# Optimization experiments

Measured on AMD Instinct MI355X. Metric: run time of the kernel, lower is better.

The kernel has to match this reference:

```python
import jax, jax.numpy as jnp
import numpy as np

D = 256
HID = 128
TOPK = 100
NEG = -20.0


def setup_inputs() -> dict:
    key = jax.random.key(0)
    ks = jax.random.split(key, 10)
    B, Ll, Lp = 2, 96, 768
    l_tok = jax.random.normal(ks[0], (B, Ll, D), dtype=jnp.float32)
    p_tok = jax.random.normal(ks[1], (B, Lp, D), dtype=jnp.float32)
    # trailing-position padding (pad last 8 ligand / 64 protein tokens)
    l_pad = jnp.broadcast_to(jnp.arange(Ll) >= Ll - 8, (B, Ll))
    p_pad = jnp.broadcast_to(jnp.arange(Lp) >= Lp - 64, (B, Lp))
    s = 0.02
    Wl = jax.random.normal(ks[2], (D, D), dtype=jnp.float32) * s
    bl = jnp.zeros((D,), jnp.float32)
    Wp = jax.random.normal(ks[3], (D, D), dtype=jnp.float32) * s
    bp = jnp.zeros((D,), jnp.float32)
    W1 = jax.random.normal(ks[4], (4 * D, HID), dtype=jnp.float32) * s
    b1 = jnp.zeros((HID,), jnp.float32)
    W2 = jax.random.normal(ks[5], (HID, HID), dtype=jnp.float32) * s
    b2 = jnp.zeros((HID,), jnp.float32)
    W3 = jax.random.normal(ks[6], (HID, 1), dtype=jnp.float32) * s
    b3 = jnp.zeros((1,), jnp.float32)
    return {"l_tok": l_tok, "p_tok": p_tok, "l_pad": l_pad, "p_pad": p_pad,
            "Wl": Wl, "bl": bl, "Wp": Wp, "bp": bp,
            "W1": W1, "b1": b1, "W2": W2, "b2": b2, "W3": W3, "b3": b3}


def _pair_head(l_tok, p_tok, l_pad, p_pad, Wl, bl, Wp, bp, W1, b1, W2, b2, W3, b3):
    B, Ll, d = l_tok.shape
    Lp = p_tok.shape[1]
    l = l_tok @ Wl + bl                      # [B,Ll,D]
    p = p_tok @ Wp + bp                      # [B,Lp,D]
    le = jnp.broadcast_to(l[:, :, None, :], (B, Ll, Lp, d))
    pe = jnp.broadcast_to(p[:, None, :, :], (B, Ll, Lp, d))
    pair = jnp.concatenate([le, pe, le * pe, jnp.abs(le - pe)], axis=-1)  # [B,Ll,Lp,4D]
    h = jax.nn.gelu(pair @ W1 + b1, approximate=False)
    h = jax.nn.gelu(h @ W2 + b2, approximate=False)
    logit_map = (h @ W3 + b3)[..., 0]        # [B,Ll,Lp]
    logit_map = jnp.nan_to_num(logit_map, nan=0.0, posinf=20.0, neginf=NEG)
    valid = (~l_pad)[:, :, None] & (~p_pad)[:, None, :]
    logit_map = jnp.where(valid, logit_map, NEG)
    flat = logit_map.reshape(B, Ll * Lp)
    k = min(TOPK, Ll * Lp)
    topv, _ = jax.lax.top_k(flat, k)
    w = jax.nn.softmax(topv, axis=-1)
    return jnp.sum(w * topv, axis=-1)        # [B]


def reference(l_tok, p_tok, l_pad, p_pad, Wl, bl, Wp, bp, W1, b1, W2, b2, W3, b3):
    return _pair_head(l_tok, p_tok, l_pad, p_pad, Wl, bl, Wp, bp, W1, b1, W2, b2, W3, b3)
```

## Files before the change

### kernel.cpp

```cpp
#include <hip/hip_runtime.h>
#include <hip/hip_bf16.h>
#include <math.h>

#define LL 96
#define LP 768
#define BD 256
#define HD 128
#define NB 2
#define NEGV (-20.0f)
#define LB 8
#define PB 16

#define NBIN 4096
#define BSHIFT 20
#define CAP 8192
#define NLOG (LL * LP)

typedef __attribute__((ext_vector_type(4))) float f32x4;
typedef __attribute__((ext_vector_type(4))) unsigned int u32x4;
typedef __attribute__((ext_vector_type(8))) short s16x8;

__device__ __forceinline__ float gelu_fast(float x) {
  float ax = fabsf(x) * 0.70710678118654752f;
  float t = __builtin_amdgcn_rcpf(fmaf(0.3275911f, ax, 1.0f));
  float poly = t * fmaf(t, fmaf(t, fmaf(t, fmaf(t, 1.061405429f, -1.453152027f),
                                        1.421413741f), -0.284496736f), 0.254829592f);
  float e = __expf(-ax * ax);
  float erfax = fmaf(-poly, e, 1.0f);
  float erfx = copysignf(erfax, x);
  return 0.5f * x * (1.0f + erfx);
}

__device__ __forceinline__ f32x4 mfma16(s16x8 a, s16x8 b, f32x4 c) {
  return __builtin_amdgcn_mfma_f32_16x16x32_bf16(a, b, c, 0, 0, 0);
}

__device__ __forceinline__ unsigned pack_bf16(float a, float b) {
  float2 t; t.x = a; t.y = b;
  __hip_bfloat162 h = __float22bfloat162_rn(t);
  return *reinterpret_cast<unsigned*>(&h);
}

__device__ __forceinline__ s16x8 as_s16x8(u32x4 v) {
  return __builtin_bit_cast(s16x8, v);
}

__device__ __forceinline__ s16x8 pack8(f32x4 x0, f32x4 x1) {
  u32x4 v;
  v[0] = pack_bf16(x0[0], x0[1]);
  v[1] = pack_bf16(x0[2], x0[3]);
  v[2] = pack_bf16(x1[0], x1[1]);
  v[3] = pack_bf16(x1[2], x1[3]);
  return as_s16x8(v);
}

__device__ __forceinline__ unsigned short bfbits(float x) {
  __hip_bfloat16 h = __float2bfloat16(x);
  return *reinterpret_cast<unsigned short*>(&h);
}

__device__ __forceinline__ unsigned int fkey(float f) {
  unsigned int u = __float_as_uint(f);
  return u ^ ((u >> 31) ? 0xFFFFFFFFu : 0x80000000u);
}
__device__ __forceinline__ float finv(unsigned int k) {
  unsigned int u = k ^ ((k >> 31) ? 0x80000000u : 0xFFFFFFFFu);
  return __uint_as_float(u);
}


__global__ __launch_bounds__(256) void prep_kernel(
    const void* lp, const void* pp, unsigned char* lmask, unsigned char* pmask,
    const float* __restrict__ W1, const float* __restrict__ W2,
    unsigned short* __restrict__ W1xf, unsigned short* __restrict__ W2f,
    const float* __restrict__ l_tok, const float* __restrict__ p_tok,
    const float* __restrict__ Wl, const float* __restrict__ bl,
    const float* __restrict__ Wp, const float* __restrict__ bp,
    const float* __restrict__ b1,
    float* __restrict__ wl_, float* __restrict__ wp_,
    float* __restrict__ wA, float* __restrict__ wB,
    unsigned* __restrict__ zero_base) {
  __shared__ int bad;
  const int tid = threadIdx.x;
  if (blockIdx.x == 0) {
    for (int i = tid; i < NB * NBIN + 32; i += 256) zero_base[i] = 0u;
    if (tid == 0) bad = 0;
    __syncthreads();
    const unsigned int* li = (const unsigned int*)lp;
    const unsigned int* pi = (const unsigned int*)pp;
    for (int i = tid; i < NB * LL; i += 256) if (li[i] > 1u) atomicOr(&bad, 1);
    for (int i = tid; i < NB * LP; i += 256) if (pi[i] > 1u) atomicOr(&bad, 1);
    __syncthreads();
    const bool asInt = (bad == 0);
    const unsigned char* lb = (const unsigned char*)lp;
    const unsigned char* pb = (const unsigned char*)pp;
    for (int i = tid; i < NB * LL; i += 256)
      lmask[i] = asInt ? (unsigned char)(li[i] != 0u) : (unsigned char)(lb[i] != 0);
    for (int i = tid; i < NB * LP; i += 256)
      pmask[i] = asInt ? (unsigned char)(pi[i] != 0u) : (unsigned char)(pb[i] != 0);
    return;
  }
  if (blockIdx.x < 321) {
    int idx = (blockIdx.x - 1) * 256 + tid;
    if (idx < 65536) {
      int j = idx & 7, ln = (idx >> 3) & 63;
      int rest = idx >> 9;
      int mt = rest & 7, kt = (rest >> 3) & 1, cc = rest >> 4;
      int row = 512 + cc * 64 + kt * 32 + ((ln >> 4) << 3) + j;
      int col = mt * 16 + (ln & 15);
      W1xf[idx] = bfbits(W1[row * HD + col]);
    } else if (idx < 65536 + 16384) {
      int e = idx - 65536;
      int j = e & 7, ln = (e >> 3) & 63, mt = (e >> 9) & 7, kt = e >> 12;
      int row = kt * 32 + ((ln >> 4) << 3) + j;
      int col = mt * 16 + (ln & 15);
      W2f[e] = bfbits(W2[row * HD + col]);
    }
    return;
  }
  const int pblk = blockIdx.x - 321;
  const bool isL = pblk < (NB * LL / 16);
  const int blk = isL ? pblk : (pblk - NB * LL / 16);
  const int r0 = blk * 16;
  const float* X = isL ? l_tok : p_tok;
  const float* W = isL ? Wl : Wp;
  const float* bias = isL ? bl : bp;
  float* Y1 = isL ? wl_ : wp_;
  float* Y2 = isL ? wA : wB;
  const float* W1p = isL ? W1 : (W1 + 256 * HD);

  const int lane = tid & 63;
  const int wv = tid >> 6;
  const int mrow = lane & 15;
  const int kg = (lane >> 4) * 8;
  const int drow = (lane >> 4) * 4;

  f32x4 accA[4];
#pragma unroll
  for (int q = 0; q < 4; ++q) {
    float bv = bias[(wv * 4 + q) * 16 + mrow];
    accA[q] = (f32x4){bv, bv, bv, bv};
  }
#pragma unroll
  for (int kt = 0; kt < 8; ++kt) {
    const float* xr = &X[(size_t)(r0 + mrow) * 256 + kt * 32 + kg];
    s16x8 af = pack8(*(const f32x4*)xr, *(const f32x4*)(xr + 4));
#pragma unroll
    for (int q = 0; q < 4; ++q) {
      const int nc = (wv * 4 + q) * 16 + mrow;
      f32x4 w0, w1;
#pragma unroll
      for (int j = 0; j < 4; ++j) {
        w0[j] = W[(size_t)(kt * 32 + kg + j) * 256 + nc];
        w1[j] = W[(size_t)(kt * 32 + kg + 4 + j) * 256 + nc];
      }
      accA[q] = mfma16(af, pack8(w0, w1), accA[q]);
    }
  }
#pragma unroll
  for (int q = 0; q < 4; ++q)
#pragma unroll
    for (int r = 0; r < 4; ++r)
      Y1[(size_t)(r0 + drow + r) * 256 + (wv * 4 + q) * 16 + mrow] = accA[q][r];
  __syncthreads();

  f32x4 accB[2];
#pragma unroll
  for (int q = 0; q < 2; ++q) {
    float bv = isL ? b1[(wv * 2 + q) * 16 + mrow] : 0.0f;
    accB[q] = (f32x4){bv, bv, bv, bv};
  }
#pragma unroll
  for (int kt = 0; kt < 8; ++kt) {
    const float* yr = &Y1[(size_t)(r0 + mrow) * 256 + kt * 32 + kg];
    s16x8 af = pack8(*(const f32x4*)yr, *(const f32x4*)(yr + 4));
#pragma unroll
    for (int q = 0; q < 2; ++q) {
      const int nc = (wv * 2 + q) * 16 + mrow;
      f32x4 w0, w1;
#pragma unroll
      for (int j = 0; j < 4; ++j) {
        w0[j] = W1p[(size_t)(kt * 32 + kg + j) * HD + nc];
        w1[j] = W1p[(size_t)(kt * 32 + kg + 4 + j) * HD + nc];
      }
      accB[q] = mfma16(af, pack8(w0, w1), accB[q]);
    }
  }
#pragma unroll
  for (int q = 0; q < 2; ++q)
#pragma unroll
    for (int r = 0; r < 4; ++r)
      Y2[(size_t)(r0 + drow + r) * HD + (wv * 2 + q) * 16 + mrow] = accB[q][r];
}

__global__ __launch_bounds__(256, 3) void pair2_kernel(
    const float* __restrict__ lbuf, const float* __restrict__ pbuf,
    const float* __restrict__ A1, const float* __restrict__ B1,
    const unsigned short* __restrict__ W1xf, const unsigned short* __restrict__ W2f,
    const float* __restrict__ b2, const float* __restrict__ W3,
    const float* __restrict__ b3, const unsigned char* __restrict__ lmask,
    const unsigned char* __restrict__ pmask, float* __restrict__ logits) {
  __shared__ float U[8192];

  const int tid = threadIdx.x;
  const int lane = tid & 63;
  const int w = tid >> 6;
  const int g = lane >> 4;
  const int c = lane & 15;
  const int bb = blockIdx.z;
  const int i0 = blockIdx.y * LB;
  const int j0 = blockIdx.x * PB;

  float* lt0 = U;
  float* lt1 = U + 1632;

  const int srow = tid >> 4, sq = tid & 15;
  const int srow2 = (tid + 256) >> 4;

  auto gaddr = [&](int row, int q, int c4) -> const float* {
    return (row < 8)
        ? &lbuf[(size_t)(bb * LL + i0 + row) * BD + c4 * 64 + q * 4]
        : &pbuf[(size_t)(bb * LP + j0 + (row - 8)) * BD + c4 * 64 + q * 4];
  };

  {
    f32x4 r0 = *(const f32x4*)gaddr(srow, sq, 0);
    f32x4 r1 = {};
    if (tid < 128) r1 = *(const f32x4*)gaddr(srow2, sq, 0);
    *(f32x4*)&lt0[srow * 68 + sq * 4] = r0;
    if (tid < 128) *(f32x4*)&lt0[srow2 * 68 + sq * 4] = r1;
  }
  __syncthreads();

  f32x4 acc1[8][2];
#pragma unroll
  for (int m = 0; m < 8; ++m)
#pragma unroll
    for (int n = 0; n < 2; ++n) acc1[m][n] = (f32x4)0.0f;

  for (int c4 = 0; c4 < 4; ++c4) {
    float* cur = (c4 & 1) ? lt1 : lt0;
    float* nxt = (c4 & 1) ? lt0 : lt1;

    f32x4 r0 = {}, r1 = {};
    if (c4 < 3) {
      r0 = *(const f32x4*)gaddr(srow, sq, c4 + 1);
      if (tid < 128) r1 = *(const f32x4*)gaddr(srow2, sq, c4 + 1);
    }

#pragma unroll
    for (int kt = 0; kt < 2; ++kt) {
      const int kc0 = kt * 32 + g * 8;
      s16x8 a0[8];
#pragma unroll
      for (int m = 0; m < 8; ++m)
        a0[m] = *(const s16x8*)(W1xf +
            ((size_t)((c4 * 2 + kt) * 8 + m) * 64 + lane) * 8);

      const f32x4 p0 = *(const f32x4*)&cur[(8 + c) * 68 + kc0];
      const f32x4 p1 = *(const f32x4*)&cur[(8 + c) * 68 + kc0 + 4];
      s16x8 bf0[2], bf1[2];
#pragma unroll
      for (int n = 0; n < 2; ++n) {
        const int ntg = w * 2 + n;
        const f32x4 l0 = *(const f32x4*)&cur[ntg * 68 + kc0];
        const f32x4 l1 = *(const f32x4*)&cur[ntg * 68 + kc0 + 4];
        u32x4 bv;
        bv[0] = pack_bf16(l0[0] * p0[0], l0[1] * p0[1]);
        bv[1] = pack_bf16(l0[2] * p0[2], l0[3] * p0[3]);
        bv[2] = pack_bf16(l1[0] * p1[0], l1[1] * p1[1]);
        bv[3] = pack_bf16(l1[2] * p1[2], l1[3] * p1[3]);
        bf0[n] = as_s16x8(bv);
      }

      s16x8 a1[8];
#pragma unroll
      for (int m = 0; m < 8; ++m)
        a1[m] = *(const s16x8*)(W1xf +
            ((size_t)(((4 + c4) * 2 + kt) * 8 + m) * 64 + lane) * 8);

#pragma unroll
      for (int n = 0; n < 2; ++n) {
        const int ntg = w * 2 + n;
        const f32x4 l0 = *(const f32x4*)&cur[ntg * 68 + kc0];
        const f32x4 l1 = *(const f32x4*)&cur[ntg * 68 + kc0 + 4];
        u32x4 bv;
        bv[0] = pack_bf16(fabsf(l0[0] - p0[0]), fabsf(l0[1] - p0[1]));
        bv[1] = pack_bf16(fabsf(l0[2] - p0[2]), fabsf(l0[3] - p0[3]));
        bv[2] = pack_bf16(fabsf(l1[0] - p1[0]), fabsf(l1[1] - p1[1]));
        bv[3] = pack_bf16(fabsf(l1[2] - p1[2]), fabsf(l1[3] - p1[3]));
        bf1[n] = as_s16x8(bv);
      }

#pragma unroll
      for (int m = 0; m < 8; ++m) {
        acc1[m][0] = mfma16(a0[m], bf0[0], acc1[m][0]);
        acc1[m][1] = mfma16(a0[m], bf0[1], acc1[m][1]);
      }
#pragma unroll
      for (int m = 0; m < 8; ++m) {
        acc1[m][0] = mfma16(a1[m], bf1[0], acc1[m][0]);
        acc1[m][1] = mfma16(a1[m], bf1[1], acc1[m][1]);
      }
    }

    if (c4 < 3) {
      *(f32x4*)&nxt[srow * 68 + sq * 4] = r0;
      if (tid < 128) *(f32x4*)&nxt[srow2 * 68 + sq * 4] = r1;
    }
    __syncthreads();
  }

  unsigned* Hdw = (unsigned*)U;
#pragma unroll
  for (int m = 0; m < 8; ++m) {
    const int kt2 = (4 * m + g) >> 3;
    const int l2 = ((2 * m + (g >> 1)) & 3) * 16 + c;
    const int jd = (g & 1) * 2;
    const f32x4 b1v = *(const f32x4*)&B1[(size_t)(bb * LP + j0 + c) * HD + m * 16 + g * 4];
#pragma unroll
    for (int n = 0; n < 2; ++n) {
      const int ntg = w * 2 + n;
      f32x4 a1v = *(const f32x4*)&A1[(size_t)(bb * LL + i0 + ntg) * HD + m * 16 + g * 4];
      float h0 = gelu_fast(acc1[m][n][0] + a1v[0] + b1v[0]);
      float h1 = gelu_fast(acc1[m][n][1] + a1v[1] + b1v[1]);
      float h2 = gelu_fast(acc1[m][n][2] + a1v[2] + b1v[2]);
      float h3 = gelu_fast(acc1[m][n][3] + a1v[3] + b1v[3]);
      uint2 hw;
      hw.x = pack_bf16(h0, h1);
      hw.y = pack_bf16(h2, h3);
      *(uint2*)&Hdw[((kt2 * 8 + ntg) * 64 + l2) * 4 + jd] = hw;
    }
  }
  __syncthreads();

  f32x4 acc2[8][2];
#pragma unroll
  for (int m = 0; m < 8; ++m)
#pragma unroll
    for (int n = 0; n < 2; ++n) acc2[m][n] = (f32x4)0.0f;

  const unsigned short* Hush = (const unsigned short*)U;
#pragma unroll
  for (int kt = 0; kt < 4; ++kt) {
    s16x8 a2[8];
#pragma unroll
    for (int m = 0; m < 8; ++m)
      a2[m] = *(const s16x8*)(W2f + (size_t)((kt * 8 + m) * 64 + lane) * 8);
    s16x8 bf[2];
#pragma unroll
    for (int n = 0; n < 2; ++n)
      bf[n] = *((const s16x8*)Hush + ((kt * 8 + (w * 2 + n)) * 64 + lane));
#pragma unroll
    for (int m = 0; m < 8; ++m) {
      acc2[m][0] = mfma16(a2[m], bf[0], acc2[m][0]);
      acc2[m][1] = mfma16(a2[m], bf[1], acc2[m][1]);
    }
  }

  float partial[2] = {0.0f, 0.0f};
#pragma unroll
  for (int m = 0; m < 8; ++m) {
    const int hb = m * 16 + g * 4;
    f32x4 b2v = *(const f32x4*)&b2[hb];
    f32x4 w3v = *(const f32x4*)&W3[hb];
#pragma unroll
    for (int n = 0; n < 2; ++n) {
#pragma unroll
      for (int r = 0; r < 4; ++r)
        partial[n] = fmaf(gelu_fast(acc2[m][n][r] + b2v[r]), w3v[r], partial[n]);
    }
  }
#pragma unroll
  for (int n = 0; n < 2; ++n) {
    partial[n] += __shfl_xor(partial[n], 16, 64);
    partial[n] += __shfl_xor(partial[n], 32, 64);
  }
  if (g == 0) {
    const float bb3 = b3[0];
#pragma unroll
    for (int n = 0; n < 2; ++n) {
      const int ntg = w * 2 + n;
      float v = partial[n] + bb3;
      if (isnan(v)) v = 0.0f;
      else if (isinf(v)) v = (v > 0.0f) ? 20.0f : NEGV;
      const int i = i0 + ntg, j = j0 + c;
      if (lmask[bb * LL + i] || pmask[bb * LP + j]) v = NEGV;
      logits[(size_t)bb * NLOG + i * LP + j] = v;
    }
  }
}

__global__ __launch_bounds__(256) void topk_kernel(const float* __restrict__ logits,
                                                   unsigned* __restrict__ hist,
                                                   unsigned* __restrict__ ctrl,
                                                   float* __restrict__ cand,
                                                   float* __restrict__ out) {
  __shared__ unsigned lh[NBIN];
  __shared__ unsigned csum[256];
  __shared__ unsigned suf[256];
  __shared__ unsigned topb[256];
  __shared__ float red[256];
  __shared__ unsigned sP, sN, isLastS;
  __shared__ unsigned bc[8];
  const int b = blockIdx.y;
  const int tid = threadIdx.x;
  const float* data = logits + (size_t)b * NLOG;
  const int stride = gridDim.x * 256;

  for (int i = tid; i < NBIN; i += 256) lh[i] = 0u;
  __syncthreads();
  for (int i = blockIdx.x * 256 + tid; i < NLOG; i += stride)
    atomicAdd(&lh[fkey(data[i]) >> BSHIFT], 1u);
  __syncthreads();
  unsigned* gh = hist + b * NBIN;
  for (int i = tid; i < NBIN; i += 256) {
    unsigned v = lh[i];
    if (v) atomicAdd(&gh[i], v);
  }
  __threadfence();
  if (tid == 0) isLastS = (atomicAdd(&ctrl[12 + b], 1u) == gridDim.x - 1);
  __syncthreads();

  if (isLastS) {
    __threadfence();
    const int base = tid * (NBIN / 256);
    unsigned s = 0;
    int top = -1;
    for (int i = 0; i < NBIN / 256; ++i) {
      unsigned cnt = gh[base + i];
      s += cnt;
      if (cnt) top = base + i;
    }
    csum[tid] = s;
    topb[tid] = (unsigned)(top + 1);
    __syncthreads();
    if (tid == 0) {
      unsigned a = 0;
      for (int t = 255; t >= 0; --t) { suf[t] = a; a += csum[t]; }
      unsigned mt = 0;
      for (int t = 0; t < 256; ++t) mt = max(mt, topb[t]);
      ctrl[b] = ((mt - 1u) << BSHIFT) | ((1u << BSHIFT) - 1u);
    }
    __syncthreads();
    unsigned above = suf[tid];
    if (above < 100u && above + csum[tid] >= 100u) {
      unsigned a = above;
      for (int i = NBIN / 256 - 1; i >= 0; --i) {
        unsigned hc = gh[base + i];
        if (a + hc >= 100u) { ctrl[4 + b] = base + i; ctrl[6 + b] = a; break; }
        a += hc;
      }
    }
    __syncthreads();
    __threadfence();
    if (tid == 0) atomicExch(&ctrl[16 + b], 1u);
  } else {
    if (tid == 0) {
      int guard = 0;
      while (atomicAdd(&ctrl[16 + b], 0u) == 0u && guard < (1 << 24)) {
        __builtin_amdgcn_s_sleep(32);
        ++guard;
      }
    }
    __syncthreads();
  }

  if (tid == 0) {
    bc[0] = atomicAdd(&ctrl[4 + b], 0u);
    bc[1] = atomicAdd(&ctrl[b], 0u);
  }
  __syncthreads();
  const unsigned B = bc[0];
  const float vmax = finv(bc[1]);

  {
    float l1 = 0.0f, l2 = 0.0f;
    for (int i = blockIdx.x * 256 + tid; i < NLOG; i += stride) {
      float v = data[i];
      unsigned kb = fkey(v) >> BSHIFT;
      if (kb > B) {
        float e = __expf(v - vmax);
        l1 += e;
        l2 = fmaf(e, v, l2);
      } else if (kb == B) {
        unsigned pos = atomicAdd(&ctrl[2 + b], 1u);
        if (pos < CAP) cand[(size_t)b * CAP + pos] = v;
      }
    }
    if (l1 != 0.0f) {
      atomicAdd((float*)&ctrl[8 + b], l1);
      atomicAdd((float*)&ctrl[10 + b], l2);
    }
  }
  __threadfence();
  if (tid == 0) isLastS = (atomicAdd(&ctrl[14 + b], 1u) == gridDim.x - 1);
  __syncthreads();
  if (!isLastS) return;
  __threadfence();

  if (tid == 0) {
    bc[2] = atomicAdd(&ctrl[2 + b], 0u);
    bc[3] = atomicAdd(&ctrl[6 + b], 0u);
    bc[4] = __float_as_uint(atomicAdd((float*)&ctrl[8 + b], 0.0f));
    bc[5] = __float_as_uint(atomicAdd((float*)&ctrl[10 + b], 0.0f));
  }
  __syncthreads();
  const unsigned count = bc[2];
  const unsigned G = bc[3];
  const float s1g = __uint_as_float(bc[4]);
  const float s2g = __uint_as_float(bc[5]);
  const float* cv = cand + (size_t)b * CAP;
  const bool fb = count > CAP;
  const unsigned C = fb ? 0u : count;

  if (tid == 0) { sP = 0u; sN = fb ? 100u : (100u - G); }
  __syncthreads();

  for (int sh = 24; sh >= 0; sh -= 8) {
    csum[tid] = 0u;
    __syncthreads();
    const unsigned prefix = sP;
    const unsigned maskhi = (sh == 24) ? 0u : (0xFFFFFFFFu << (sh + 8));
    if (!fb) {
      for (int i = tid; i < (int)C; i += 256) {
        unsigned k = fkey(cv[i]);
        if ((k & maskhi) == (prefix & maskhi)) atomicAdd(&csum[(k >> sh) & 255], 1u);
      }
    } else {
      for (int i = tid; i < NLOG; i += 256) {
        unsigned k = fkey(data[i]);
        if ((k & maskhi) == (prefix & maskhi)) atomicAdd(&csum[(k >> sh) & 255], 1u);
      }
    }
    __syncthreads();
    if (tid == 0) {
      unsigned need = sN, cum = 0u;
      int d = 0;
      for (d = 255; d >= 0; --d) { cum += csum[d]; if (cum >= need) break; }
      sN = need - (cum - csum[d]);
      sP = prefix | ((unsigned)d << sh);
    }
    __syncthreads();
  }
  const unsigned Tkey = sP;
  const unsigned nT = sN;
  const float T = finv(Tkey);

  float l1 = 0.0f, l2 = 0.0f;
  if (!fb) {
    for (int i = tid; i < (int)C; i += 256) {
      float v = cv[i];
      if (fkey(v) > Tkey) { float e = __expf(v - vmax); l1 += e; l2 = fmaf(e, v, l2); }
    }
  } else {
    for (int i = tid; i < NLOG; i += 256) {
      float v = data[i];
      if (fkey(v) > Tkey) { float e = __expf(v - vmax); l1 += e; l2 = fmaf(e, v, l2); }
    }
  }
  red[tid] = l1;
  __syncthreads();
  for (int s = 128; s > 0; s >>= 1) { if (tid < s) red[tid] += red[tid + s]; __syncthreads(); }
  const float s1c = red[0];
  __syncthreads();
  red[tid] = l2;
  __syncthreads();
  for (int s = 128; s > 0; s >>= 1) { if (tid < s) red[tid] += red[tid + s]; __syncthreads(); }
  if (tid == 0) {
    const float s2c = red[0];
    const float e = __expf(T - vmax);
    const float g1 = fb ? 0.0f : s1g;
    const float g2 = fb ? 0.0f : s2g;
    const float denom = g1 + s1c + (float)nT * e;
    const float num = g2 + s2c + (float)nT * e * T;
    out[b] = num / denom;
  }
}

extern "C" void kernel_launch(void* const* d_in, const int* in_sizes, int n_in,
                              void* d_out, int out_size, void* d_ws, size_t ws_size,
                              hipStream_t stream) {
  const float* l_tok = (const float*)d_in[0];
  const float* p_tok = (const float*)d_in[1];
  const void* l_pad = d_in[2];
  const void* p_pad = d_in[3];
  const float* Wl = (const float*)d_in[4];
  const float* bl = (const float*)d_in[5];
  const float* Wp = (const float*)d_in[6];
  const float* bp = (const float*)d_in[7];
  const float* W1 = (const float*)d_in[8];
  const float* b1 = (const float*)d_in[9];
  const float* W2 = (const float*)d_in[10];
  const float* b2 = (const float*)d_in[11];
  const float* W3 = (const float*)d_in[12];
  const float* b3 = (const float*)d_in[13];

  float* ws = (float*)d_ws;
  float* wl_ = ws;
  float* wp_ = ws + 49152;
  float* wA = ws + 442368;
  float* wB = ws + 466944;
  float* wLog = ws + 663552;
  unsigned char* lmask = (unsigned char*)(ws + 811008);
  unsigned char* pmask = lmask + NB * LL;
  unsigned short* W1xf = (unsigned short*)(ws + 811520);
  unsigned short* W2f = (unsigned short*)(ws + 844288);
  unsigned* hist = (unsigned*)(ws + 852480);
  unsigned* ctrl = (unsigned*)(ws + 852480 + NB * NBIN);
  float* cand = ws + 852480 + NB * NBIN + 32;

  prep_kernel<<<321 + NB * (LL + LP) / 16, 256, 0, stream>>>(
      l_pad, p_pad, lmask, pmask, W1, W2, W1xf, W2f,
      l_tok, p_tok, Wl, bl, Wp, bp, b1, wl_, wp_, wA, wB, hist);

  dim3 grid(LP / PB, LL / LB, NB);
  pair2_kernel<<<grid, 256, 0, stream>>>(wl_, wp_, wA, wB, W1xf, W2f,
                                         b2, W3, b3, lmask, pmask, wLog);
  topk_kernel<<<dim3(32, NB), 256, 0, stream>>>(wLog, hist, ctrl, cand,
                                                (float*)d_out);
}
```

Baseline: 121.2 us.

## Pre-swizzle projection weights to bf16 and split prep into swizzle and projection kernels

The Wl/Wp projection weights and the first two W1 blocks are now converted to bf16 and stored in MFMA fragment order by a separate swizzle kernel. A new projection kernel then loads each B fragment with one 16-byte vector load instead of eight strided scalar fp32 loads plus packing. This cuts the uncoalesced global loads in the projection GEMMs. The cost is an extra kernel launch and a serial dependency between swizzle and projection, where the old single prep kernel ran them side by side.

After: 122.0 us. No clear change (+0.7%).

```diff
diff --git a/kernel.cpp b/kernel.cpp
--- a/kernel.cpp
+++ b/kernel.cpp
@@ -69,17 +69,13 @@
 }
 
 
-__global__ __launch_bounds__(256) void prep_kernel(
+__global__ __launch_bounds__(256) void swz_kernel(
     const void* lp, const void* pp, unsigned char* lmask, unsigned char* pmask,
     const float* __restrict__ W1, const float* __restrict__ W2,
+    const float* __restrict__ Wl, const float* __restrict__ Wp,
     unsigned short* __restrict__ W1xf, unsigned short* __restrict__ W2f,
-    const float* __restrict__ l_tok, const float* __restrict__ p_tok,
-    const float* __restrict__ Wl, const float* __restrict__ bl,
-    const float* __restrict__ Wp, const float* __restrict__ bp,
-    const float* __restrict__ b1,
-    float* __restrict__ wl_, float* __restrict__ wp_,
-    float* __restrict__ wA, float* __restrict__ wB,
-    unsigned* __restrict__ zero_base) {
+    unsigned short* __restrict__ Wlf, unsigned short* __restrict__ Wpf,
+    unsigned short* __restrict__ W1abf, unsigned* __restrict__ zero_base) {
   __shared__ int bad;
   const int tid = threadIdx.x;
   if (blockIdx.x == 0) {
@@ -100,34 +96,60 @@
       pmask[i] = asInt ? (unsigned char)(pi[i] != 0u) : (unsigned char)(pb[i] != 0);
     return;
   }
-  if (blockIdx.x < 321) {
-    int idx = (blockIdx.x - 1) * 256 + tid;
-    if (idx < 65536) {
-      int j = idx & 7, ln = (idx >> 3) & 63;
-      int rest = idx >> 9;
-      int mt = rest & 7, kt = (rest >> 3) & 1, cc = rest >> 4;
-      int row = 512 + cc * 64 + kt * 32 + ((ln >> 4) << 3) + j;
-      int col = mt * 16 + (ln & 15);
-      W1xf[idx] = bfbits(W1[row * HD + col]);
-    } else if (idx < 65536 + 16384) {
-      int e = idx - 65536;
-      int j = e & 7, ln = (e >> 3) & 63, mt = (e >> 9) & 7, kt = e >> 12;
-      int row = kt * 32 + ((ln >> 4) << 3) + j;
-      int col = mt * 16 + (ln & 15);
-      W2f[e] = bfbits(W2[row * HD + col]);
-    }
-    return;
-  }
-  const int pblk = blockIdx.x - 321;
-  const bool isL = pblk < (NB * LL / 16);
-  const int blk = isL ? pblk : (pblk - NB * LL / 16);
+  int idx = (blockIdx.x - 1) * 256 + tid;
+  if (idx < 65536) {
+    int j = idx & 7, ln = (idx >> 3) & 63;
+    int rest = idx >> 9;
+    int mt = rest & 7, kt = (rest >> 3) & 1, cc = rest >> 4;
+    int row = 512 + cc * 64 + kt * 32 + ((ln >> 4) << 3) + j;
+    int col = mt * 16 + (ln & 15);
+    W1xf[idx] = bfbits(W1[row * HD + col]);
+  } else if (idx < 81920) {
+    int e = idx - 65536;
+    int j = e & 7, ln = (e >> 3) & 63, mt = (e >> 9) & 7, kt = e >> 12;
+    int row = kt * 32 + ((ln >> 4) << 3) + j;
+    int col = mt * 16 + (ln & 15);
+    W2f[e] = bfbits(W2[row * HD + col]);
+  } else if (idx < 147456) {
+    int e = idx - 81920;
+    int j = e & 7, ln = (e >> 3) & 63, nt = (e >> 9) & 15, kt = e >> 13;
+    int row = kt * 32 + ((ln >> 4) << 3) + j;
+    int col = nt * 16 + (ln & 15);
+    Wlf[e] = bfbits(Wl[row * 256 + col]);
+  } else if (idx < 212992) {
+    int e = idx - 147456;
+    int j = e & 7, ln = (e >> 3) & 63, nt = (e >> 9) & 15, kt = e >> 13;
+    int row = kt * 32 + ((ln >> 4) << 3) + j;
+    int col = nt * 16 + (ln & 15);
+    Wpf[e] = bfbits(Wp[row * 256 + col]);
+  } else if (idx < 278528) {
+    int e = idx - 212992;
+    int j = e & 7, ln = (e >> 3) & 63, nt = (e >> 9) & 7, kt = (e >> 12) & 7;
+    int part = e >> 15;
+    int row = part * 256 + kt * 32 + ((ln >> 4) << 3) + j;
+    int col = nt * 16 + (ln & 15);
+    W1abf[e] = bfbits(W1[row * HD + col]);
+  }
+}
+
+__global__ __launch_bounds__(256) void proj_kernel(
+    const float* __restrict__ l_tok, const float* __restrict__ p_tok,
+    const unsigned short* __restrict__ Wlf, const unsigned short* __restrict__ Wpf,
+    const unsigned short* __restrict__ W1abf,
+    const float* __restrict__ bl, const float* __restrict__ bp,
+    const float* __restrict__ b1,
+    float* __restrict__ wl_, float* __restrict__ wp_,
+    float* __restrict__ wA, float* __restrict__ wB) {
+  const int tid = threadIdx.x;
+  const bool isL = blockIdx.x < (NB * LL / 16);
+  const int blk = isL ? blockIdx.x : (blockIdx.x - NB * LL / 16);
   const int r0 = blk * 16;
   const float* X = isL ? l_tok : p_tok;
-  const float* W = isL ? Wl : Wp;
+  const unsigned short* Wf = isL ? Wlf : Wpf;
   const float* bias = isL ? bl : bp;
   float* Y1 = isL ? wl_ : wp_;
   float* Y2 = isL ? wA : wB;
-  const float* W1p = isL ? W1 : (W1 + 256 * HD);
+  const unsigned short* Wab = W1abf + (isL ? 0 : 32768);
 
   const int lane = tid & 63;
   const int wv = tid >> 6;
@@ -147,14 +169,9 @@
     s16x8 af = pack8(*(const f32x4*)xr, *(const f32x4*)(xr + 4));
 #pragma unroll
     for (int q = 0; q < 4; ++q) {
-      const int nc = (wv * 4 + q) * 16 + mrow;
-      f32x4 w0, w1;
-#pragma unroll
-      for (int j = 0; j < 4; ++j) {
-        w0[j] = W[(size_t)(kt * 32 + kg + j) * 256 + nc];
-        w1[j] = W[(size_t)(kt * 32 + kg + 4 + j) * 256 + nc];
-      }
-      accA[q] = mfma16(af, pack8(w0, w1), accA[q]);
+      const int nt = wv * 4 + q;
+      s16x8 bf = *(const s16x8*)(Wf + ((size_t)((kt * 16 + nt) * 64 + lane)) * 8);
+      accA[q] = mfma16(af, bf, accA[q]);
     }
   }
 #pragma unroll
@@ -176,14 +193,9 @@
     s16x8 af = pack8(*(const f32x4*)yr, *(const f32x4*)(yr + 4));
 #pragma unroll
     for (int q = 0; q < 2; ++q) {
-      const int nc = (wv * 2 + q) * 16 + mrow;
-      f32x4 w0, w1;
-#pragma unroll
-      for (int j = 0; j < 4; ++j) {
-        w0[j] = W1p[(size_t)(kt * 32 + kg + j) * HD + nc];
-        w1[j] = W1p[(size_t)(kt * 32 + kg + 4 + j) * HD + nc];
-      }
-      accB[q] = mfma16(af, pack8(w0, w1), accB[q]);
+      const int nt = wv * 2 + q;
+      s16x8 bf = *(const s16x8*)(Wab + ((size_t)((kt * 8 + nt) * 64 + lane)) * 8);
+      accB[q] = mfma16(af, bf, accB[q]);
     }
   }
 #pragma unroll
@@ -609,10 +621,16 @@
   unsigned* hist = (unsigned*)(ws + 852480);
   unsigned* ctrl = (unsigned*)(ws + 852480 + NB * NBIN);
   float* cand = ws + 852480 + NB * NBIN + 32;
-
-  prep_kernel<<<321 + NB * (LL + LP) / 16, 256, 0, stream>>>(
-      l_pad, p_pad, lmask, pmask, W1, W2, W1xf, W2f,
-      l_tok, p_tok, Wl, bl, Wp, bp, b1, wl_, wp_, wA, wB, hist);
+  unsigned short* Wlf = (unsigned short*)(ws + 877088);
+  unsigned short* Wpf = (unsigned short*)(ws + 909856);
+  unsigned short* W1abf = (unsigned short*)(ws + 942624);
+
+  swz_kernel<<<1 + 278528 / 256, 256, 0, stream>>>(
+      l_pad, p_pad, lmask, pmask, W1, W2, Wl, Wp,
+      W1xf, W2f, Wlf, Wpf, W1abf, hist);
+
+  proj_kernel<<<NB * (LL + LP) / 16, 256, 0, stream>>>(
+      l_tok, p_tok, Wlf, Wpf, W1abf, bl, bp, b1, wl_, wp_, wA, wB);
 
   dim3 grid(LP / PB, LL / LB, NB);
   pair2_kernel<<<grid, 256, 0, stream>>>(wl_, wp_, wA, wB, W1xf, W2f,
```

## Fuse logit histogram into pair kernel and drop top-k spin-wait phase

Applied to the files above, without the earlier changes.

Each pair-kernel block now builds a shared-memory histogram of the logits it writes and atomically merges it into the global histogram. The top-k kernel therefore no longer re-reads all logits for a histogram pass and no longer needs the last-block election and spin-wait before candidate selection. Every top-k block recomputes the threshold bin directly from the finished global histogram, and the top-k grid is widened from 32 to 64 blocks per batch. In exchange, each of the many pair blocks clears a 4096-bin shared histogram and scans it for global atomics, which adds extra syncs and work to that kernel's tail.

Result: faster. 114.7 us (-5.3%).

```diff
diff --git a/kernel.cpp b/kernel.cpp
--- a/kernel.cpp
+++ b/kernel.cpp
@@ -199,7 +199,8 @@
     const unsigned short* __restrict__ W1xf, const unsigned short* __restrict__ W2f,
     const float* __restrict__ b2, const float* __restrict__ W3,
     const float* __restrict__ b3, const unsigned char* __restrict__ lmask,
-    const unsigned char* __restrict__ pmask, float* __restrict__ logits) {
+    const unsigned char* __restrict__ pmask, float* __restrict__ logits,
+    unsigned* __restrict__ hist) {
   __shared__ float U[8192];
 
   const int tid = threadIdx.x;
@@ -376,55 +377,65 @@
     partial[n] += __shfl_xor(partial[n], 16, 64);
     partial[n] += __shfl_xor(partial[n], 32, 64);
   }
-  if (g == 0) {
+  const bool writer = (g == 0);
+  float vv0 = NEGV, vv1 = NEGV;
+  if (writer) {
     const float bb3 = b3[0];
-#pragma unroll
-    for (int n = 0; n < 2; ++n) {
-      const int ntg = w * 2 + n;
-      float v = partial[n] + bb3;
+    {
+      float v = partial[0] + bb3;
       if (isnan(v)) v = 0.0f;
       else if (isinf(v)) v = (v > 0.0f) ? 20.0f : NEGV;
-      const int i = i0 + ntg, j = j0 + c;
+      const int i = i0 + w * 2, j = j0 + c;
       if (lmask[bb * LL + i] || pmask[bb * LP + j]) v = NEGV;
       logits[(size_t)bb * NLOG + i * LP + j] = v;
-    }
-  }
-}
-
-__global__ __launch_bounds__(256) void topk_kernel(const float* __restrict__ logits,
-                                                   unsigned* __restrict__ hist,
-                                                   unsigned* __restrict__ ctrl,
-                                                   float* __restrict__ cand,
-                                                   float* __restrict__ out) {
-  __shared__ unsigned lh[NBIN];
+      vv0 = v;
+    }
+    {
+      float v = partial[1] + bb3;
+      if (isnan(v)) v = 0.0f;
+      else if (isinf(v)) v = (v > 0.0f) ? 20.0f : NEGV;
+      const int i = i0 + w * 2 + 1, j = j0 + c;
+      if (lmask[bb * LL + i] || pmask[bb * LP + j]) v = NEGV;
+      logits[(size_t)bb * NLOG + i * LP + j] = v;
+      vv1 = v;
+    }
+  }
+
+  unsigned* lh = (unsigned*)U;
+  __syncthreads();
+  for (int i = tid; i < NBIN; i += 256) lh[i] = 0u;
+  __syncthreads();
+  if (writer) {
+    atomicAdd(&lh[fkey(vv0) >> BSHIFT], 1u);
+    atomicAdd(&lh[fkey(vv1) >> BSHIFT], 1u);
+  }
+  __syncthreads();
+  unsigned* gh = hist + bb * NBIN;
+  for (int i = tid; i < NBIN; i += 256) {
+    unsigned v = lh[i];
+    if (v) atomicAdd(&gh[i], v);
+  }
+}
+
+__global__ __launch_bounds__(256) void topk2_kernel(const float* __restrict__ logits,
+                                                    const unsigned* __restrict__ hist,
+                                                    unsigned* __restrict__ ctrl,
+                                                    float* __restrict__ cand,
+                                                    float* __restrict__ out) {
   __shared__ unsigned csum[256];
   __shared__ unsigned suf[256];
   __shared__ unsigned topb[256];
   __shared__ float red[256];
-  __shared__ unsigned sP, sN, isLastS;
-  __shared__ unsigned bc[8];
+  __shared__ unsigned sB, sG, sUB, sP, sN, isLastS;
+  __shared__ unsigned bc[4];
   const int b = blockIdx.y;
   const int tid = threadIdx.x;
   const float* data = logits + (size_t)b * NLOG;
+  const unsigned* gh = hist + b * NBIN;
   const int stride = gridDim.x * 256;
 
-  for (int i = tid; i < NBIN; i += 256) lh[i] = 0u;
-  __syncthreads();
-  for (int i = blockIdx.x * 256 + tid; i < NLOG; i += stride)
-    atomicAdd(&lh[fkey(data[i]) >> BSHIFT], 1u);
-  __syncthreads();
-  unsigned* gh = hist + b * NBIN;
-  for (int i = tid; i < NBIN; i += 256) {
-    unsigned v = lh[i];
-    if (v) atomicAdd(&gh[i], v);
-  }
-  __threadfence();
-  if (tid == 0) isLastS = (atomicAdd(&ctrl[12 + b], 1u) == gridDim.x - 1);
-  __syncthreads();
-
-  if (isLastS) {
-    __threadfence();
-    const int base = tid * (NBIN / 256);
+  const int base = tid * (NBIN / 256);
+  {
     unsigned s = 0;
     int top = -1;
     for (int i = 0; i < NBIN / 256; ++i) {
@@ -434,45 +445,31 @@
     }
     csum[tid] = s;
     topb[tid] = (unsigned)(top + 1);
-    __syncthreads();
-    if (tid == 0) {
-      unsigned a = 0;
-      for (int t = 255; t >= 0; --t) { suf[t] = a; a += csum[t]; }
-      unsigned mt = 0;
-      for (int t = 0; t < 256; ++t) mt = max(mt, topb[t]);
-      ctrl[b] = ((mt - 1u) << BSHIFT) | ((1u << BSHIFT) - 1u);
-    }
-    __syncthreads();
+  }
+  __syncthreads();
+  if (tid == 0) {
+    unsigned a = 0;
+    for (int t = 255; t >= 0; --t) { suf[t] = a; a += csum[t]; }
+    unsigned mt = 0;
+    for (int t = 0; t < 256; ++t) mt = max(mt, topb[t]);
+    sUB = ((mt - 1u) << BSHIFT) | ((1u << BSHIFT) - 1u);
+  }
+  __syncthreads();
+  {
     unsigned above = suf[tid];
     if (above < 100u && above + csum[tid] >= 100u) {
       unsigned a = above;
       for (int i = NBIN / 256 - 1; i >= 0; --i) {
         unsigned hc = gh[base + i];
-        if (a + hc >= 100u) { ctrl[4 + b] = base + i; ctrl[6 + b] = a; break; }
+        if (a + hc >= 100u) { sB = base + i; sG = a; break; }
         a += hc;
       }
     }
-    __syncthreads();
-    __threadfence();
-    if (tid == 0) atomicExch(&ctrl[16 + b], 1u);
-  } else {
-    if (tid == 0) {
-      int guard = 0;
-      while (atomicAdd(&ctrl[16 + b], 0u) == 0u && guard < (1 << 24)) {
-        __builtin_amdgcn_s_sleep(32);
-        ++guard;
-      }
-    }
-    __syncthreads();
-  }
-
-  if (tid == 0) {
-    bc[0] = atomicAdd(&ctrl[4 + b], 0u);
-    bc[1] = atomicAdd(&ctrl[b], 0u);
-  }
-  __syncthreads();
-  const unsigned B = bc[0];
-  const float vmax = finv(bc[1]);
+  }
+  __syncthreads();
+  const unsigned B = sB;
+  const unsigned G = sG;
+  const float vmax = finv(sUB);
 
   {
     float l1 = 0.0f, l2 = 0.0f;
@@ -500,16 +497,14 @@
   __threadfence();
 
   if (tid == 0) {
-    bc[2] = atomicAdd(&ctrl[2 + b], 0u);
-    bc[3] = atomicAdd(&ctrl[6 + b], 0u);
-    bc[4] = __float_as_uint(atomicAdd((float*)&ctrl[8 + b], 0.0f));
-    bc[5] = __float_as_uint(atomicAdd((float*)&ctrl[10 + b], 0.0f));
-  }
-  __syncthreads();
-  const unsigned count = bc[2];
-  const unsigned G = bc[3];
-  const float s1g = __uint_as_float(bc[4]);
-  const float s2g = __uint_as_float(bc[5]);
+    bc[0] = atomicAdd(&ctrl[2 + b], 0u);
+    bc[1] = __float_as_uint(atomicAdd((float*)&ctrl[8 + b], 0.0f));
+    bc[2] = __float_as_uint(atomicAdd((float*)&ctrl[10 + b], 0.0f));
+  }
+  __syncthreads();
+  const unsigned count = bc[0];
+  const float s1g = __uint_as_float(bc[1]);
+  const float s2g = __uint_as_float(bc[2]);
   const float* cv = cand + (size_t)b * CAP;
   const bool fb = count > CAP;
   const unsigned C = fb ? 0u : count;
@@ -616,7 +611,8 @@
 
   dim3 grid(LP / PB, LL / LB, NB);
   pair2_kernel<<<grid, 256, 0, stream>>>(wl_, wp_, wA, wB, W1xf, W2f,
-                                         b2, W3, b3, lmask, pmask, wLog);
-  topk_kernel<<<dim3(32, NB), 256, 0, stream>>>(wLog, hist, ctrl, cand,
-                                                (float*)d_out);
-}
+                                         b2, W3, b3, lmask, pmask, wLog, hist);
+
+  topk2_kernel<<<dim3(64, NB), 256, 0, stream>>>(wLog, hist, ctrl, cand,
+                                                 (float*)d_out);
+}
```
